# Kernel tuning notes

Measured on AMD Instinct MI355X. Metric: run time of the kernel, lower is better.

The kernel has to match this reference:

```python
import jax, jax.numpy as jnp
import numpy as np

HID = 70
NL = 4
NCLS = 10
BN_EPS = 1e-5

def _linear_params(key, din, dout):
    k1, k2 = jax.random.split(key)
    s = 1.0 / np.sqrt(din)
    W = jax.random.uniform(k1, (din, dout), jnp.float32, -s, s)
    b = jax.random.uniform(k2, (dout,), jnp.float32, -s, s)
    return W, b

def setup_inputs():
    key = jax.random.key(0)
    N, E, IN = 100000, 500000, 128
    keys = jax.random.split(key, 64)
    it = iter(keys)
    inp = {}
    inp['h'] = jax.random.normal(next(it), (N, IN), jnp.float32)
    inp['e'] = jax.random.normal(next(it), (E, IN), jnp.float32)
    inp['src'] = jax.random.randint(next(it), (E,), 0, N)
    inp['dst'] = jax.random.randint(next(it), (E,), 0, N)
    inp['snorm_n'] = jax.random.uniform(next(it), (N,), jnp.float32, 0.05, 1.0)
    inp['snorm_e'] = jax.random.uniform(next(it), (E,), jnp.float32, 0.05, 1.0)
    inp['W_eh'], inp['b_eh'] = _linear_params(next(it), IN, HID)
    inp['W_ee'], inp['b_ee'] = _linear_params(next(it), IN, HID)
    for nm in ['A', 'B', 'C', 'D', 'E']:
        Ws, bs = [], []
        for _ in range(NL):
            W, b = _linear_params(next(it), HID, HID)
            Ws.append(W); bs.append(b)
        inp['W' + nm] = jnp.stack(Ws)  # [NL, HID, HID]
        inp['b' + nm] = jnp.stack(bs)  # [NL, HID]
    inp['bnh_g'] = jnp.ones((NL, HID), jnp.float32)
    inp['bnh_b'] = jnp.zeros((NL, HID), jnp.float32)
    inp['bne_g'] = jnp.ones((NL, HID), jnp.float32)
    inp['bne_b'] = jnp.zeros((NL, HID), jnp.float32)
    inp['W_m0'], inp['b_m0'] = _linear_params(next(it), HID, HID // 2)
    inp['W_m1'], inp['b_m1'] = _linear_params(next(it), HID // 2, HID // 4)
    inp['W_m2'], inp['b_m2'] = _linear_params(next(it), HID // 4, NCLS)
    return inp

def _bn(x, g, b):
    # training-mode batch norm over the node/edge dimension
    m = jnp.mean(x, 0)
    v = jnp.var(x, 0)
    return (x - m) * jax.lax.rsqrt(v + BN_EPS) * g + b

def _forward(h, e, snorm_n, snorm_e, W_eh, b_eh, W_ee, b_ee, WA, bA, WB, bB, WC, bC, WD, bD, WE, bE, bnh_g, bnh_b, bne_g, bne_b, W_m0, b_m0, W_m1, b_m1, W_m2, b_m2, src, dst):
    N = h.shape[0]
    snn = snorm_n[:, None]
    sne = snorm_e[:, None]
    h = h @ W_eh + b_eh  # [N, HID]
    e = e @ W_ee + b_ee  # [E, HID]
    for l in range(NL):
        h_in, e_in = h, e
        Ah = h @ WA[l] + bA[l]
        Bh = h @ WB[l] + bB[l]
        Dh = h @ WD[l] + bD[l]
        Eh = h @ WE[l] + bE[l]
        Ce = e @ WC[l] + bC[l]
        e_hat = Ce + Dh[src] + Eh[dst]  # [E, HID] gated edge features
        sigma = jax.nn.sigmoid(e_hat)
        num = jax.ops.segment_sum(sigma * Bh[src], dst, num_segments=N)
        den = jax.ops.segment_sum(sigma, dst, num_segments=N)
        h = Ah + num / (den + 1e-6)
        h = _bn(h * snn, bnh_g[l], bnh_b[l])
        e = _bn(e_hat * sne, bne_g[l], bne_b[l])
        h = h_in + jax.nn.relu(h)  # residual
        e = e_in + jax.nn.relu(e)
    # MLPReadout: 70 -> 35 -> 17 -> n_classes
    y = jax.nn.relu(h @ W_m0 + b_m0)
    y = jax.nn.relu(y @ W_m1 + b_m1)
    return y @ W_m2 + b_m2

def reference(h, e, src, dst, snorm_n, snorm_e, W_eh, b_eh, W_ee, b_ee, WA, bA, WB, bB, WC, bC, WD, bD, WE, bE, bnh_g, bnh_b, bne_g, bne_b, W_m0, b_m0, W_m1, b_m1, W_m2, b_m2):
    return _forward(h, e, snorm_n, snorm_e, W_eh, b_eh, W_ee, b_ee, WA, bA, WB, bB, WC, bC, WD, bD, WE, bE, bnh_g, bnh_b, bne_g, bne_b, W_m0, b_m0, W_m1, b_m1, W_m2, b_m2, src, dst)
```

## Files before the change

kernel.cpp:

```cpp
#include <hip/hip_runtime.h>
#include <math.h>

#define H 70
#define NLAY 4
#define NCLS 10

typedef __attribute__((ext_vector_type(8))) short bf16x8;
typedef __attribute__((ext_vector_type(4))) float f32x4;
typedef __attribute__((ext_vector_type(4))) unsigned int uint4v;
typedef __attribute__((ext_vector_type(4))) int int4v;

struct GemmMats {
    const float* w[4];
    const float* b[4];
    float* y[4];
};

__device__ inline unsigned pack_hi16(unsigned u0, unsigned u1) {
    return (u1 & 0xFFFF0000u) | (u0 >> 16);
}
__device__ inline void split_pair(float x0, float x1, unsigned& ph, unsigned& pl) {
    unsigned u0 = __float_as_uint(x0), u1 = __float_as_uint(x1);
    float l0 = x0 - __uint_as_float(u0 & 0xFFFF0000u);
    float l1 = x1 - __uint_as_float(u1 & 0xFFFF0000u);
    ph = pack_hi16(u0, u1);
    pl = pack_hi16(__float_as_uint(l0), __float_as_uint(l1));
}

template <int K, int NMAT>
__global__ __launch_bounds__(256) void gemm_mfma(const float* __restrict__ X,
                                                 int M, GemmMats P) {
    constexpr int KS = (K + 31) / 32;
    constexpr int JK = KS * 16;
    constexpr int SW = JK + 4;
    __shared__ unsigned int Wsh[2 * 80 * SW];

    const int tid = threadIdx.x;
    const int wv = tid >> 6;
    const int lane = tid & 63;
    const int mlane = lane & 15;
    const int q = lane >> 4;
    const int rowbase = blockIdx.x * 64 + wv * 16;
    const int rowc = min(rowbase + mlane, M - 1);

    bf16x8 Ah[KS], Al[KS];
    {
        const float* xr = X + (size_t)rowc * K;
#pragma unroll
        for (int ks = 0; ks < KS; ++ks) {
            int k0 = ks * 32 + q * 8;
            float x[8];
            if (k0 + 8 <= K) {
                float2 p0 = *(const float2*)(xr + k0);
                float2 p1 = *(const float2*)(xr + k0 + 2);
                float2 p2 = *(const float2*)(xr + k0 + 4);
                float2 p3 = *(const float2*)(xr + k0 + 6);
                x[0] = p0.x; x[1] = p0.y; x[2] = p1.x; x[3] = p1.y;
                x[4] = p2.x; x[5] = p2.y; x[6] = p3.x; x[7] = p3.y;
            } else {
#pragma unroll
                for (int j = 0; j < 8; ++j)
                    x[j] = (k0 + j < K) ? xr[k0 + j] : 0.f;
            }
            int4v vh, vl;
            unsigned ph, pl;
            split_pair(x[0], x[1], ph, pl); vh.x = ph; vl.x = pl;
            split_pair(x[2], x[3], ph, pl); vh.y = ph; vl.y = pl;
            split_pair(x[4], x[5], ph, pl); vh.z = ph; vl.z = pl;
            split_pair(x[6], x[7], ph, pl); vh.w = ph; vl.w = pl;
            Ah[ks] = __builtin_bit_cast(bf16x8, vh);
            Al[ks] = __builtin_bit_cast(bf16x8, vl);
        }
    }

    for (int m = 0; m < NMAT; ++m) {
        __syncthreads();
        const float* Wg = P.w[m];
        for (int idx = tid; idx < 80 * JK; idx += 256) {
            int n = idx / JK, j = idx - n * JK;
            int k0 = 2 * j;
            float w0 = (n < H && k0 < K) ? Wg[k0 * H + n] : 0.f;
            float w1 = (n < H && k0 + 1 < K) ? Wg[(k0 + 1) * H + n] : 0.f;
            unsigned ph, pl;
            split_pair(w0, w1, ph, pl);
            Wsh[n * SW + j] = ph;
            Wsh[80 * SW + n * SW + j] = pl;
        }
        __syncthreads();

        f32x4 acc[5];
#pragma unroll
        for (int nt = 0; nt < 5; ++nt) acc[nt] = {0.f, 0.f, 0.f, 0.f};

#pragma unroll
        for (int ks = 0; ks < KS; ++ks) {
#pragma unroll
            for (int nt = 0; nt < 5; ++nt) {
                int base = (nt * 16 + mlane) * SW + ks * 16 + q * 4;
                uint4v bhv = *(const uint4v*)&Wsh[base];
                uint4v blv = *(const uint4v*)&Wsh[80 * SW + base];
                bf16x8 Bh = __builtin_bit_cast(bf16x8, bhv);
                bf16x8 Bl = __builtin_bit_cast(bf16x8, blv);
                acc[nt] = __builtin_amdgcn_mfma_f32_16x16x32_bf16(Ah[ks], Bh, acc[nt], 0, 0, 0);
                acc[nt] = __builtin_amdgcn_mfma_f32_16x16x32_bf16(Al[ks], Bh, acc[nt], 0, 0, 0);
                acc[nt] = __builtin_amdgcn_mfma_f32_16x16x32_bf16(Ah[ks], Bl, acc[nt], 0, 0, 0);
            }
        }

        const float* bm = P.b[m];
        float* Ym = P.y[m];
#pragma unroll
        for (int nt = 0; nt < 5; ++nt) {
            int col = nt * 16 + mlane;
            if (col < H) {
                float bv = bm[col];
#pragma unroll
                for (int r = 0; r < 4; ++r) {
                    int grow = rowbase + q * 4 + r;
                    if (grow < M)
                        Ym[(size_t)grow * H + col] = acc[nt][r] + bv;
                }
            }
        }
    }
}

__global__ void count_deg(const int* __restrict__ dst, int E,
                          int* __restrict__ deg) {
    int e = blockIdx.x * 256 + threadIdx.x;
    if (e < E) atomicAdd(&deg[dst[e]], 1);
}

__global__ __launch_bounds__(256) void scan_phaseA(const int* __restrict__ deg,
                                                   int N, int* __restrict__ bsum) {
    __shared__ int red[256];
    int base = blockIdx.x * 1024;
    int s = 0;
    for (int i = threadIdx.x; i < 1024; i += 256) {
        int g = base + i;
        if (g < N) s += deg[g];
    }
    red[threadIdx.x] = s;
    __syncthreads();
    for (int off = 128; off > 0; off >>= 1) {
        if (threadIdx.x < off) red[threadIdx.x] += red[threadIdx.x + off];
        __syncthreads();
    }
    if (threadIdx.x == 0) bsum[blockIdx.x] = red[0];
}

__global__ void scan_phaseB(const int* __restrict__ bsum, int NB,
                            int* __restrict__ boff, int* __restrict__ rowstart,
                            int N) {
    if (threadIdx.x == 0 && blockIdx.x == 0) {
        int acc = 0;
        for (int i = 0; i < NB; ++i) {
            boff[i] = acc;
            acc += bsum[i];
        }
        rowstart[N] = acc;
    }
}

__global__ __launch_bounds__(256) void scan_phaseC(
    const int* __restrict__ deg, int N, const int* __restrict__ boff,
    int* __restrict__ rowstart, int* __restrict__ cursor) {
    __shared__ int thr[256];
    int base = blockIdx.x * 1024 + threadIdx.x * 4;
    int d[4], loc[4];
    int s = 0;
#pragma unroll
    for (int i = 0; i < 4; ++i) {
        int g = base + i;
        d[i] = (g < N) ? deg[g] : 0;
        loc[i] = s;
        s += d[i];
    }
    thr[threadIdx.x] = s;
    __syncthreads();
    if (threadIdx.x == 0) {
        int a = 0;
        for (int i = 0; i < 256; ++i) {
            int t = thr[i];
            thr[i] = a;
            a += t;
        }
    }
    __syncthreads();
    int off = boff[blockIdx.x] + thr[threadIdx.x];
#pragma unroll
    for (int i = 0; i < 4; ++i) {
        int g = base + i;
        if (g < N) {
            rowstart[g] = off + loc[i];
            cursor[g] = off + loc[i];
        }
    }
}

__global__ void csr_fill(const int* __restrict__ dst, int E,
                         int* __restrict__ cursor, int* __restrict__ eid) {
    int e = blockIdx.x * 256 + threadIdx.x;
    if (e < E) {
        int p = atomicAdd(&cursor[dst[e]], 1);
        eid[p] = e;
    }
}

__global__ __launch_bounds__(256) void edge_kernel(
    float* __restrict__ ehat, const float* __restrict__ Dh,
    const float* __restrict__ Eh, const int* __restrict__ src,
    const int* __restrict__ dst, const float* __restrict__ sne, int E,
    float* __restrict__ esum, float* __restrict__ esq) {
    __shared__ float ls[H], lq[H];
    for (int i = threadIdx.x; i < H; i += 256) {
        ls[i] = 0.f;
        lq[i] = 0.f;
    }
    __syncthreads();
    const int total = E * H;
    const int stride = gridDim.x * 256;
    int idx0 = blockIdx.x * 256 + threadIdx.x;
    const int c = idx0 % H;
    float s1 = 0.f, s2 = 0.f;
    for (int idx = idx0; idx < total; idx += stride) {
        int e = idx / H;
        int s = src[e], d = dst[e];
        float v = ehat[idx] + Dh[s * H + c] + Eh[d * H + c];
        ehat[idx] = v;
        float t = v * sne[e];
        s1 += t;
        s2 += t * t;
    }
    atomicAdd(&ls[c], s1);
    atomicAdd(&lq[c], s2);
    __syncthreads();
    for (int i = threadIdx.x; i < H; i += 256) {
        unsafeAtomicAdd(&esum[i], ls[i]);
        unsafeAtomicAdd(&esq[i], lq[i]);
    }
}

__global__ void bn_finalize(const float* __restrict__ stats, float inv_cnt,
                            const float* __restrict__ g,
                            const float* __restrict__ b,
                            float* __restrict__ scale,
                            float* __restrict__ shift) {
    int c = threadIdx.x;
    if (c < H) {
        float m = stats[c] * inv_cnt;
        float v = stats[H + c] * inv_cnt - m * m;
        float rs = rsqrtf(v + 1e-5f);
        float sc = g[c] * rs;
        scale[c] = sc;
        shift[c] = b[c] - m * sc;
    }
}

__global__ __launch_bounds__(256) void update_kernel(
    float* __restrict__ io, const float* __restrict__ pre,
    const float* __restrict__ rowscale, const float* __restrict__ scale,
    const float* __restrict__ shift, int total) {
    const int stride = gridDim.x * 256;
    for (int idx = blockIdx.x * 256 + threadIdx.x; idx < total; idx += stride) {
        int r = idx / H;
        int c = idx - r * H;
        float t = pre[idx];
        if (rowscale) t *= rowscale[r];
        io[idx] += fmaxf(fmaf(t, scale[c], shift[c]), 0.f);
    }
}

__global__ __launch_bounds__(256) void node_agg(
    const float* __restrict__ ehat, const float* __restrict__ Bh,
    const float* __restrict__ Ah, const int* __restrict__ src,
    const int* __restrict__ rowstart, const int* __restrict__ eid,
    const float* __restrict__ snn, int N, float* __restrict__ hpre,
    float* __restrict__ hsum, float* __restrict__ hsq) {
    __shared__ float ls[H], lq[H];
    for (int i = threadIdx.x; i < H; i += 256) {
        ls[i] = 0.f;
        lq[i] = 0.f;
    }
    __syncthreads();
    const int total = N * H;
    const int stride = gridDim.x * 256;
    int idx0 = blockIdx.x * 256 + threadIdx.x;
    const int c = idx0 % H;
    float s1 = 0.f, s2 = 0.f;
    for (int idx = idx0; idx < total; idx += stride) {
        int n = idx / H;
        int p0 = rowstart[n], p1 = rowstart[n + 1];
        float num = 0.f, den = 0.f;
        for (int p = p0; p < p1; ++p) {
            int ed = eid[p];
            float x = ehat[ed * H + c];
            float sg = 1.f / (1.f + __expf(-x));
            den += sg;
            num = fmaf(sg, Bh[src[ed] * H + c], num);
        }
        float val = (Ah[idx] + num / (den + 1e-6f)) * snn[n];
        hpre[idx] = val;
        s1 += val;
        s2 += val * val;
    }
    atomicAdd(&ls[c], s1);
    atomicAdd(&lq[c], s2);
    __syncthreads();
    for (int i = threadIdx.x; i < H; i += 256) {
        unsafeAtomicAdd(&hsum[i], ls[i]);
        unsafeAtomicAdd(&hsq[i], lq[i]);
    }
}

__global__ __launch_bounds__(128) void mlp_readout(
    const float* __restrict__ h, int M, const float* __restrict__ W0,
    const float* __restrict__ b0, const float* __restrict__ W1,
    const float* __restrict__ b1, const float* __restrict__ W2,
    const float* __restrict__ b2, float* __restrict__ out) {
    __shared__ float Hs[128 * 71];
    __shared__ float wbuf[70 * 35 + 35 + 35 * 17 + 17 + 17 * 10 + 10];
    float* sW0 = wbuf;
    float* sb0 = sW0 + 2450;
    float* sW1 = sb0 + 35;
    float* sb1 = sW1 + 595;
    float* sW2 = sb1 + 17;
    float* sb2 = sW2 + 170;
    int tid = threadIdx.x;
    for (int i = tid; i < 2450; i += 128) sW0[i] = W0[i];
    for (int i = tid; i < 35; i += 128) sb0[i] = b0[i];
    for (int i = tid; i < 595; i += 128) sW1[i] = W1[i];
    for (int i = tid; i < 17; i += 128) sb1[i] = b1[i];
    for (int i = tid; i < 170; i += 128) sW2[i] = W2[i];
    for (int i = tid; i < 10; i += 128) sb2[i] = b2[i];
    int row0 = blockIdx.x * 128;
    for (int idx = tid; idx < 128 * H; idx += 128) {
        int r = idx / H, k = idx - r * H;
        int g = row0 + r;
        Hs[r * 71 + k] = (g < M) ? h[(size_t)g * H + k] : 0.f;
    }
    __syncthreads();
    int n = row0 + tid;
    if (n < M) {
        float y0[35];
#pragma unroll
        for (int j = 0; j < 35; ++j) y0[j] = sb0[j];
        for (int k = 0; k < H; ++k) {
            float x = Hs[tid * 71 + k];
#pragma unroll
            for (int j = 0; j < 35; ++j) y0[j] = fmaf(x, sW0[k * 35 + j], y0[j]);
        }
#pragma unroll
        for (int j = 0; j < 35; ++j) y0[j] = fmaxf(y0[j], 0.f);
        float y1[17];
#pragma unroll
        for (int j = 0; j < 17; ++j) y1[j] = sb1[j];
        for (int k = 0; k < 35; ++k) {
            float x = y0[k];
#pragma unroll
            for (int j = 0; j < 17; ++j) y1[j] = fmaf(x, sW1[k * 17 + j], y1[j]);
        }
#pragma unroll
        for (int j = 0; j < 17; ++j) y1[j] = fmaxf(y1[j], 0.f);
        float y2[10];
#pragma unroll
        for (int j = 0; j < 10; ++j) y2[j] = sb2[j];
        for (int k = 0; k < 17; ++k) {
            float x = y1[k];
#pragma unroll
            for (int j = 0; j < 10; ++j) y2[j] = fmaf(x, sW2[k * 10 + j], y2[j]);
        }
#pragma unroll
        for (int j = 0; j < 10; ++j) out[(size_t)n * 10 + j] = y2[j];
    }
}

extern "C" void kernel_launch(void* const* d_in, const int* in_sizes, int n_in,
                              void* d_out, int out_size, void* d_ws,
                              size_t ws_size, hipStream_t stream) {
    const float* in_h = (const float*)d_in[0];
    const float* in_e = (const float*)d_in[1];
    const int* src = (const int*)d_in[2];
    const int* dst = (const int*)d_in[3];
    const float* snn = (const float*)d_in[4];
    const float* sne = (const float*)d_in[5];
    const float* W_eh = (const float*)d_in[6];
    const float* b_eh = (const float*)d_in[7];
    const float* W_ee = (const float*)d_in[8];
    const float* b_ee = (const float*)d_in[9];
    const float* WA = (const float*)d_in[10];
    const float* bA = (const float*)d_in[11];
    const float* WB = (const float*)d_in[12];
    const float* bB = (const float*)d_in[13];
    const float* WC = (const float*)d_in[14];
    const float* bC = (const float*)d_in[15];
    const float* WD = (const float*)d_in[16];
    const float* bD = (const float*)d_in[17];
    const float* WE = (const float*)d_in[18];
    const float* bE = (const float*)d_in[19];
    const float* bnh_g = (const float*)d_in[20];
    const float* bnh_b = (const float*)d_in[21];
    const float* bne_g = (const float*)d_in[22];
    const float* bne_b = (const float*)d_in[23];
    const float* W_m0 = (const float*)d_in[24];
    const float* b_m0 = (const float*)d_in[25];
    const float* W_m1 = (const float*)d_in[26];
    const float* b_m1 = (const float*)d_in[27];
    const float* W_m2 = (const float*)d_in[28];
    const float* b_m2 = (const float*)d_in[29];

    const int N = in_sizes[0] / 128;
    const int E = in_sizes[1] / 128;
    const size_t nh = (size_t)N * H;
    const size_t ne = (size_t)E * H;

    float* p = (float*)d_ws;
    float* h_cur = p;   p += nh;
    float* e_cur = p;   p += ne;
    float* Ah = p;      p += nh;
    float* Bh = p;      p += nh;
    float* Dh = p;      p += nh;
    float* Eh = p;      p += nh;
    float* ehat = p;    p += ne;
    float* stats = p;   p += 280;
    float* escale = p;  p += H;
    float* eshift = p;  p += H;
    float* hscale = p;  p += H;
    float* hshift = p;  p += H;
    int* ip = (int*)p;
    int* deg = ip;      ip += N;
    int* rowstart = ip; ip += N + 1;
    int* cursor = ip;   ip += N;
    int* eid = ip;      ip += E;
    int* bsum = ip;     ip += 256;
    int* boff = ip;     ip += 256;
    float* hpre = Dh;

    hipMemsetAsync(deg, 0, (size_t)N * sizeof(int), stream);
    count_deg<<<(E + 255) / 256, 256, 0, stream>>>(dst, E, deg);
    const int NB = (N + 1023) / 1024;
    scan_phaseA<<<NB, 256, 0, stream>>>(deg, N, bsum);
    scan_phaseB<<<1, 64, 0, stream>>>(bsum, NB, boff, rowstart, N);
    scan_phaseC<<<NB, 256, 0, stream>>>(deg, N, boff, rowstart, cursor);
    csr_fill<<<(E + 255) / 256, 256, 0, stream>>>(dst, E, cursor, eid);

    GemmMats Ph = {};
    Ph.w[0] = W_eh; Ph.b[0] = b_eh; Ph.y[0] = h_cur;
    gemm_mfma<128, 1><<<(N + 63) / 64, 256, 0, stream>>>(in_h, N, Ph);
    GemmMats Pe = {};
    Pe.w[0] = W_ee; Pe.b[0] = b_ee; Pe.y[0] = e_cur;
    gemm_mfma<128, 1><<<(E + 63) / 64, 256, 0, stream>>>(in_e, E, Pe);

    for (int l = 0; l < NLAY; ++l) {
        GemmMats P4;
        P4.w[0] = WA + l * H * H; P4.b[0] = bA + l * H; P4.y[0] = Ah;
        P4.w[1] = WB + l * H * H; P4.b[1] = bB + l * H; P4.y[1] = Bh;
        P4.w[2] = WD + l * H * H; P4.b[2] = bD + l * H; P4.y[2] = Dh;
        P4.w[3] = WE + l * H * H; P4.b[3] = bE + l * H; P4.y[3] = Eh;
        gemm_mfma<70, 4><<<(N + 63) / 64, 256, 0, stream>>>(h_cur, N, P4);

        GemmMats PC = {};
        PC.w[0] = WC + l * H * H; PC.b[0] = bC + l * H; PC.y[0] = ehat;
        gemm_mfma<70, 1><<<(E + 63) / 64, 256, 0, stream>>>(e_cur, E, PC);

        hipMemsetAsync(stats, 0, 280 * sizeof(float), stream);
        edge_kernel<<<1120, 256, 0, stream>>>(ehat, Dh, Eh, src, dst, sne, E,
                                              stats, stats + 70);
        bn_finalize<<<1, 128, 0, stream>>>(stats, 1.f / E, bne_g + l * H,
                                           bne_b + l * H, escale, eshift);
        update_kernel<<<4096, 256, 0, stream>>>(e_cur, ehat, sne, escale,
                                                eshift, E * H);
        node_agg<<<1120, 256, 0, stream>>>(ehat, Bh, Ah, src, rowstart, eid,
                                           snn, N, hpre, stats + 140,
                                           stats + 210);
        bn_finalize<<<1, 128, 0, stream>>>(stats + 140, 1.f / N, bnh_g + l * H,
                                           bnh_b + l * H, hscale, hshift);
        update_kernel<<<2048, 256, 0, stream>>>(h_cur, hpre, nullptr, hscale,
                                                hshift, N * H);
    }

    mlp_readout<<<(N + 127) / 128, 128, 0, stream>>>(
        h_cur, N, W_m0, b_m0, W_m1, b_m1, W_m2, b_m2, (float*)d_out);
}
```

Measured before the change: 3.583 ms.

## Sort edges by destination, fuse edge GEMM with gating and BN stats, fuse edge update into aggregation

Edges are permuted into dst-sorted CSR order once, by gathering the initial edge GEMM input through eid and building permuted src/dst/snorm arrays, so node aggregation reads ehat contiguously. The C-projection GEMM now also adds Dh[src]+Eh[dst], writes ehat and accumulates BN statistics in one persistent kernel. The edge residual update is folded into node aggregation, and BN partial sums are spread across multiple buffers to reduce atomic contention. This removes several full passes over E×H edge tensors, but the fused GEMM epilogue now does scattered gathers and the output stays in permuted edge order.

```diff
diff --git a/kernel.cpp b/kernel.cpp
--- a/kernel.cpp
+++ b/kernel.cpp
@@ -27,8 +27,58 @@
     pl = pack_hi16(__float_as_uint(l0), __float_as_uint(l1));
 }
 
+template <int K, int KS>
+__device__ inline void load_a_frags(const float* __restrict__ X,
+                                    const int* __restrict__ perm, int M,
+                                    int rowbase, int mlane, int q,
+                                    bf16x8* Ah, bf16x8* Al) {
+    int rowc = min(rowbase + mlane, M - 1);
+    if (perm) rowc = perm[rowc];
+    const float* xr = X + (size_t)rowc * K;
+#pragma unroll
+    for (int ks = 0; ks < KS; ++ks) {
+        int k0 = ks * 32 + q * 8;
+        float x[8];
+        if (k0 + 8 <= K) {
+            float2 p0 = *(const float2*)(xr + k0);
+            float2 p1 = *(const float2*)(xr + k0 + 2);
+            float2 p2 = *(const float2*)(xr + k0 + 4);
+            float2 p3 = *(const float2*)(xr + k0 + 6);
+            x[0] = p0.x; x[1] = p0.y; x[2] = p1.x; x[3] = p1.y;
+            x[4] = p2.x; x[5] = p2.y; x[6] = p3.x; x[7] = p3.y;
+        } else {
+#pragma unroll
+            for (int j = 0; j < 8; ++j) x[j] = (k0 + j < K) ? xr[k0 + j] : 0.f;
+        }
+        int4v vh, vl;
+        unsigned ph, pl;
+        split_pair(x[0], x[1], ph, pl); vh.x = ph; vl.x = pl;
+        split_pair(x[2], x[3], ph, pl); vh.y = ph; vl.y = pl;
+        split_pair(x[4], x[5], ph, pl); vh.z = ph; vl.z = pl;
+        split_pair(x[6], x[7], ph, pl); vh.w = ph; vl.w = pl;
+        Ah[ks] = __builtin_bit_cast(bf16x8, vh);
+        Al[ks] = __builtin_bit_cast(bf16x8, vl);
+    }
+}
+
+template <int K, int JK, int SW>
+__device__ inline void stage_w(const float* __restrict__ Wg, unsigned* Wsh,
+                               int tid) {
+    for (int idx = tid; idx < 80 * JK; idx += 256) {
+        int n = idx / JK, j = idx - n * JK;
+        int k0 = 2 * j;
+        float w0 = (n < H && k0 < K) ? Wg[k0 * H + n] : 0.f;
+        float w1 = (n < H && k0 + 1 < K) ? Wg[(k0 + 1) * H + n] : 0.f;
+        unsigned ph, pl;
+        split_pair(w0, w1, ph, pl);
+        Wsh[n * SW + j] = ph;
+        Wsh[80 * SW + n * SW + j] = pl;
+    }
+}
+
 template <int K, int NMAT>
 __global__ __launch_bounds__(256) void gemm_mfma(const float* __restrict__ X,
+                                                 const int* __restrict__ perm,
                                                  int M, GemmMats P) {
     constexpr int KS = (K + 31) / 32;
     constexpr int JK = KS * 16;
@@ -41,57 +91,18 @@
     const int mlane = lane & 15;
     const int q = lane >> 4;
     const int rowbase = blockIdx.x * 64 + wv * 16;
-    const int rowc = min(rowbase + mlane, M - 1);
 
     bf16x8 Ah[KS], Al[KS];
-    {
-        const float* xr = X + (size_t)rowc * K;
-#pragma unroll
-        for (int ks = 0; ks < KS; ++ks) {
-            int k0 = ks * 32 + q * 8;
-            float x[8];
-            if (k0 + 8 <= K) {
-                float2 p0 = *(const float2*)(xr + k0);
-                float2 p1 = *(const float2*)(xr + k0 + 2);
-                float2 p2 = *(const float2*)(xr + k0 + 4);
-                float2 p3 = *(const float2*)(xr + k0 + 6);
-                x[0] = p0.x; x[1] = p0.y; x[2] = p1.x; x[3] = p1.y;
-                x[4] = p2.x; x[5] = p2.y; x[6] = p3.x; x[7] = p3.y;
-            } else {
-#pragma unroll
-                for (int j = 0; j < 8; ++j)
-                    x[j] = (k0 + j < K) ? xr[k0 + j] : 0.f;
-            }
-            int4v vh, vl;
-            unsigned ph, pl;
-            split_pair(x[0], x[1], ph, pl); vh.x = ph; vl.x = pl;
-            split_pair(x[2], x[3], ph, pl); vh.y = ph; vl.y = pl;
-            split_pair(x[4], x[5], ph, pl); vh.z = ph; vl.z = pl;
-            split_pair(x[6], x[7], ph, pl); vh.w = ph; vl.w = pl;
-            Ah[ks] = __builtin_bit_cast(bf16x8, vh);
-            Al[ks] = __builtin_bit_cast(bf16x8, vl);
-        }
-    }
+    load_a_frags<K, KS>(X, perm, M, rowbase, mlane, q, Ah, Al);
 
     for (int m = 0; m < NMAT; ++m) {
         __syncthreads();
-        const float* Wg = P.w[m];
-        for (int idx = tid; idx < 80 * JK; idx += 256) {
-            int n = idx / JK, j = idx - n * JK;
-            int k0 = 2 * j;
-            float w0 = (n < H && k0 < K) ? Wg[k0 * H + n] : 0.f;
-            float w1 = (n < H && k0 + 1 < K) ? Wg[(k0 + 1) * H + n] : 0.f;
-            unsigned ph, pl;
-            split_pair(w0, w1, ph, pl);
-            Wsh[n * SW + j] = ph;
-            Wsh[80 * SW + n * SW + j] = pl;
-        }
+        stage_w<K, JK, SW>(P.w[m], Wsh, tid);
         __syncthreads();
 
         f32x4 acc[5];
 #pragma unroll
         for (int nt = 0; nt < 5; ++nt) acc[nt] = {0.f, 0.f, 0.f, 0.f};
-
 #pragma unroll
         for (int ks = 0; ks < KS; ++ks) {
 #pragma unroll
@@ -99,14 +110,13 @@
                 int base = (nt * 16 + mlane) * SW + ks * 16 + q * 4;
                 uint4v bhv = *(const uint4v*)&Wsh[base];
                 uint4v blv = *(const uint4v*)&Wsh[80 * SW + base];
-                bf16x8 Bh = __builtin_bit_cast(bf16x8, bhv);
-                bf16x8 Bl = __builtin_bit_cast(bf16x8, blv);
-                acc[nt] = __builtin_amdgcn_mfma_f32_16x16x32_bf16(Ah[ks], Bh, acc[nt], 0, 0, 0);
-                acc[nt] = __builtin_amdgcn_mfma_f32_16x16x32_bf16(Al[ks], Bh, acc[nt], 0, 0, 0);
-                acc[nt] = __builtin_amdgcn_mfma_f32_16x16x32_bf16(Ah[ks], Bl, acc[nt], 0, 0, 0);
+                bf16x8 Bhf = __builtin_bit_cast(bf16x8, bhv);
+                bf16x8 Blf = __builtin_bit_cast(bf16x8, blv);
+                acc[nt] = __builtin_amdgcn_mfma_f32_16x16x32_bf16(Ah[ks], Bhf, acc[nt], 0, 0, 0);
+                acc[nt] = __builtin_amdgcn_mfma_f32_16x16x32_bf16(Al[ks], Bhf, acc[nt], 0, 0, 0);
+                acc[nt] = __builtin_amdgcn_mfma_f32_16x16x32_bf16(Ah[ks], Blf, acc[nt], 0, 0, 0);
             }
         }
-
         const float* bm = P.b[m];
         float* Ym = P.y[m];
 #pragma unroll
@@ -120,6 +130,108 @@
                     if (grow < M)
                         Ym[(size_t)grow * H + col] = acc[nt][r] + bv;
                 }
+            }
+        }
+    }
+}
+
+__global__ __launch_bounds__(256) void gemmC_edge(
+    const float* __restrict__ Xe, int E, const float* __restrict__ Wg,
+    const float* __restrict__ bias, const float* __restrict__ Dh,
+    const float* __restrict__ Eh, const int* __restrict__ src_p,
+    const int* __restrict__ dst_p, const float* __restrict__ sne_p,
+    float* __restrict__ ehat, float* __restrict__ estats) {
+    constexpr int K = 70, KS = 3, JK = 48, SW = 52;
+    __shared__ unsigned int Wsh[2 * 80 * SW];
+    const int tid = threadIdx.x;
+    const int wv = tid >> 6;
+    const int lane = tid & 63;
+    const int mlane = lane & 15;
+    const int q = lane >> 4;
+
+    stage_w<K, JK, SW>(Wg, Wsh, tid);
+    __syncthreads();
+
+    float bv[5];
+#pragma unroll
+    for (int nt = 0; nt < 5; ++nt) {
+        int col = nt * 16 + mlane;
+        bv[nt] = (col < H) ? bias[col] : 0.f;
+    }
+
+    float s1[5] = {0.f, 0.f, 0.f, 0.f, 0.f};
+    float s2[5] = {0.f, 0.f, 0.f, 0.f, 0.f};
+
+    const int ntiles = (E + 63) / 64;
+    for (int tile = blockIdx.x; tile < ntiles; tile += gridDim.x) {
+        const int rowbase = tile * 64 + wv * 16;
+        bf16x8 Ah[KS], Al[KS];
+        load_a_frags<K, KS>(Xe, nullptr, E, rowbase, mlane, q, Ah, Al);
+
+        f32x4 acc[5];
+#pragma unroll
+        for (int nt = 0; nt < 5; ++nt) acc[nt] = {0.f, 0.f, 0.f, 0.f};
+#pragma unroll
+        for (int ks = 0; ks < KS; ++ks) {
+#pragma unroll
+            for (int nt = 0; nt < 5; ++nt) {
+                int base = (nt * 16 + mlane) * SW + ks * 16 + q * 4;
+                uint4v bhv = *(const uint4v*)&Wsh[base];
+                uint4v blv = *(const uint4v*)&Wsh[80 * SW + base];
+                bf16x8 Bhf = __builtin_bit_cast(bf16x8, bhv);
+                bf16x8 Blf = __builtin_bit_cast(bf16x8, blv);
+                acc[nt] = __builtin_amdgcn_mfma_f32_16x16x32_bf16(Ah[ks], Bhf, acc[nt], 0, 0, 0);
+                acc[nt] = __builtin_amdgcn_mfma_f32_16x16x32_bf16(Al[ks], Bhf, acc[nt], 0, 0, 0);
+                acc[nt] = __builtin_amdgcn_mfma_f32_16x16x32_bf16(Ah[ks], Blf, acc[nt], 0, 0, 0);
+            }
+        }
+        int s4[4], d4[4];
+        float sn4[4];
+        bool ok4[4];
+#pragma unroll
+        for (int r = 0; r < 4; ++r) {
+            int grow = rowbase + q * 4 + r;
+            bool ok = grow < E;
+            int gc = ok ? grow : 0;
+            s4[r] = src_p[gc];
+            d4[r] = dst_p[gc];
+            sn4[r] = sne_p[gc];
+            ok4[r] = ok;
+        }
+#pragma unroll
+        for (int nt = 0; nt < 5; ++nt) {
+            int col = nt * 16 + mlane;
+            if (col < H) {
+#pragma unroll
+                for (int r = 0; r < 4; ++r) {
+                    if (ok4[r]) {
+                        int grow = rowbase + q * 4 + r;
+                        float v = acc[nt][r] + bv[nt] + Dh[s4[r] * H + col] +
+                                  Eh[d4[r] * H + col];
+                        ehat[(size_t)grow * H + col] = v;
+                        float t = v * sn4[r];
+                        s1[nt] += t;
+                        s2[nt] += t * t;
+                    }
+                }
+            }
+        }
+    }
+#pragma unroll
+    for (int nt = 0; nt < 5; ++nt) {
+        s1[nt] += __shfl_xor(s1[nt], 16);
+        s1[nt] += __shfl_xor(s1[nt], 32);
+        s2[nt] += __shfl_xor(s2[nt], 16);
+        s2[nt] += __shfl_xor(s2[nt], 32);
+    }
+    if (q == 0) {
+        float* buf = estats + (size_t)(blockIdx.x & 63) * 140;
+#pragma unroll
+        for (int nt = 0; nt < 5; ++nt) {
+            int col = nt * 16 + mlane;
+            if (col < H) {
+                unsafeAtomicAdd(&buf[col], s1[nt]);
+                unsafeAtomicAdd(&buf[70 + col], s2[nt]);
             }
         }
     }
@@ -207,109 +319,94 @@
     }
 }
 
-__global__ __launch_bounds__(256) void edge_kernel(
-    float* __restrict__ ehat, const float* __restrict__ Dh,
-    const float* __restrict__ Eh, const int* __restrict__ src,
-    const int* __restrict__ dst, const float* __restrict__ sne, int E,
-    float* __restrict__ esum, float* __restrict__ esq) {
-    __shared__ float ls[H], lq[H];
-    for (int i = threadIdx.x; i < H; i += 256) {
-        ls[i] = 0.f;
-        lq[i] = 0.f;
-    }
-    __syncthreads();
-    const int total = E * H;
-    const int stride = gridDim.x * 256;
-    int idx0 = blockIdx.x * 256 + threadIdx.x;
-    const int c = idx0 % H;
-    float s1 = 0.f, s2 = 0.f;
-    for (int idx = idx0; idx < total; idx += stride) {
-        int e = idx / H;
-        int s = src[e], d = dst[e];
-        float v = ehat[idx] + Dh[s * H + c] + Eh[d * H + c];
-        ehat[idx] = v;
-        float t = v * sne[e];
-        s1 += t;
-        s2 += t * t;
-    }
-    atomicAdd(&ls[c], s1);
-    atomicAdd(&lq[c], s2);
-    __syncthreads();
-    for (int i = threadIdx.x; i < H; i += 256) {
-        unsafeAtomicAdd(&esum[i], ls[i]);
-        unsafeAtomicAdd(&esq[i], lq[i]);
-    }
-}
-
-__global__ void bn_finalize(const float* __restrict__ stats, float inv_cnt,
-                            const float* __restrict__ g,
-                            const float* __restrict__ b,
-                            float* __restrict__ scale,
-                            float* __restrict__ shift) {
-    int c = threadIdx.x;
-    if (c < H) {
-        float m = stats[c] * inv_cnt;
-        float v = stats[H + c] * inv_cnt - m * m;
+__global__ void perm_build(const int* __restrict__ eid,
+                           const int* __restrict__ src,
+                           const int* __restrict__ dst,
+                           const float* __restrict__ sne, int E,
+                           int* __restrict__ src_p, int* __restrict__ dst_p,
+                           float* __restrict__ sne_p) {
+    int p = blockIdx.x * 256 + threadIdx.x;
+    if (p < E) {
+        int e = eid[p];
+        src_p[p] = src[e];
+        dst_p[p] = dst[e];
+        sne_p[p] = sne[e];
+    }
+}
+
+__global__ void bn_finalize_multi(const float* __restrict__ buf, int C,
+                                  float inv_cnt, const float* __restrict__ g,
+                                  const float* __restrict__ b,
+                                  float* __restrict__ scale,
+                                  float* __restrict__ shift) {
+    __shared__ float red[140];
+    int t = threadIdx.x;
+    if (t < 140) {
+        float s = 0.f;
+        for (int i = 0; i < C; ++i) s += buf[(size_t)i * 140 + t];
+        red[t] = s;
+    }
+    __syncthreads();
+    if (t < H) {
+        float m = red[t] * inv_cnt;
+        float v = red[70 + t] * inv_cnt - m * m;
         float rs = rsqrtf(v + 1e-5f);
-        float sc = g[c] * rs;
-        scale[c] = sc;
-        shift[c] = b[c] - m * sc;
-    }
-}
-
-__global__ __launch_bounds__(256) void update_kernel(
-    float* __restrict__ io, const float* __restrict__ pre,
-    const float* __restrict__ rowscale, const float* __restrict__ scale,
-    const float* __restrict__ shift, int total) {
-    const int stride = gridDim.x * 256;
-    for (int idx = blockIdx.x * 256 + threadIdx.x; idx < total; idx += stride) {
-        int r = idx / H;
-        int c = idx - r * H;
-        float t = pre[idx];
-        if (rowscale) t *= rowscale[r];
-        io[idx] += fmaxf(fmaf(t, scale[c], shift[c]), 0.f);
-    }
-}
-
-__global__ __launch_bounds__(256) void node_agg(
+        float sc = g[t] * rs;
+        scale[t] = sc;
+        shift[t] = b[t] - m * sc;
+    }
+}
+
+__global__ __launch_bounds__(256) void node_agg_fused(
     const float* __restrict__ ehat, const float* __restrict__ Bh,
-    const float* __restrict__ Ah, const int* __restrict__ src,
-    const int* __restrict__ rowstart, const int* __restrict__ eid,
-    const float* __restrict__ snn, int N, float* __restrict__ hpre,
-    float* __restrict__ hsum, float* __restrict__ hsq) {
-    __shared__ float ls[H], lq[H];
-    for (int i = threadIdx.x; i < H; i += 256) {
-        ls[i] = 0.f;
-        lq[i] = 0.f;
-    }
-    __syncthreads();
+    const float* __restrict__ Ah, const int* __restrict__ src_p,
+    const int* __restrict__ rowstart, const float* __restrict__ snn,
+    float* __restrict__ e_cur, const float* __restrict__ sne_p,
+    const float* __restrict__ escale, const float* __restrict__ eshift, int N,
+    float* __restrict__ hpre, float* __restrict__ hstats) {
     const int total = N * H;
     const int stride = gridDim.x * 256;
     int idx0 = blockIdx.x * 256 + threadIdx.x;
     const int c = idx0 % H;
+    const float esc = escale[c], esh = eshift[c];
     float s1 = 0.f, s2 = 0.f;
     for (int idx = idx0; idx < total; idx += stride) {
         int n = idx / H;
         int p0 = rowstart[n], p1 = rowstart[n + 1];
         float num = 0.f, den = 0.f;
         for (int p = p0; p < p1; ++p) {
-            int ed = eid[p];
-            float x = ehat[ed * H + c];
+            size_t ei = (size_t)p * H + c;
+            float x = ehat[ei];
             float sg = 1.f / (1.f + __expf(-x));
             den += sg;
-            num = fmaf(sg, Bh[src[ed] * H + c], num);
+            int s = src_p[p];
+            num = fmaf(sg, Bh[s * H + c], num);
+            e_cur[ei] += fmaxf(fmaf(x * sne_p[p], esc, esh), 0.f);
         }
         float val = (Ah[idx] + num / (den + 1e-6f)) * snn[n];
         hpre[idx] = val;
         s1 += val;
         s2 += val * val;
     }
+    __shared__ float ls[140];
+    for (int i = threadIdx.x; i < 140; i += 256) ls[i] = 0.f;
+    __syncthreads();
     atomicAdd(&ls[c], s1);
-    atomicAdd(&lq[c], s2);
-    __syncthreads();
-    for (int i = threadIdx.x; i < H; i += 256) {
-        unsafeAtomicAdd(&hsum[i], ls[i]);
-        unsafeAtomicAdd(&hsq[i], lq[i]);
+    atomicAdd(&ls[70 + c], s2);
+    __syncthreads();
+    float* buf = hstats + (size_t)(blockIdx.x & 15) * 140;
+    for (int i = threadIdx.x; i < 140; i += 256) unsafeAtomicAdd(&buf[i], ls[i]);
+}
+
+__global__ __launch_bounds__(256) void update_h_kernel(
+    float* __restrict__ io, const float* __restrict__ pre,
+    const float* __restrict__ scale, const float* __restrict__ shift,
+    int total) {
+    const int stride = gridDim.x * 256;
+    for (int idx = blockIdx.x * 256 + threadIdx.x; idx < total; idx += stride) {
+        int r = idx / H;
+        int c = idx - r * H;
+        io[idx] += fmaxf(fmaf(pre[idx], scale[c], shift[c]), 0.f);
     }
 }
 
@@ -422,19 +519,24 @@
     float* Dh = p;      p += nh;
     float* Eh = p;      p += nh;
     float* ehat = p;    p += ne;
-    float* stats = p;   p += 280;
+    float* stats = p;   p += 80 * 140;
     float* escale = p;  p += H;
     float* eshift = p;  p += H;
     float* hscale = p;  p += H;
     float* hshift = p;  p += H;
+    float* sne_p = p;   p += E;
     int* ip = (int*)p;
     int* deg = ip;      ip += N;
     int* rowstart = ip; ip += N + 1;
     int* cursor = ip;   ip += N;
     int* eid = ip;      ip += E;
+    int* src_p = ip;    ip += E;
+    int* dst_p = ip;    ip += E;
     int* bsum = ip;     ip += 256;
     int* boff = ip;     ip += 256;
     float* hpre = Dh;
+    float* estats = stats;
+    float* hstats = stats + 64 * 140;
 
     hipMemsetAsync(deg, 0, (size_t)N * sizeof(int), stream);
     count_deg<<<(E + 255) / 256, 256, 0, stream>>>(dst, E, deg);
@@ -443,13 +545,15 @@
     scan_phaseB<<<1, 64, 0, stream>>>(bsum, NB, boff, rowstart, N);
     scan_phaseC<<<NB, 256, 0, stream>>>(deg, N, boff, rowstart, cursor);
     csr_fill<<<(E + 255) / 256, 256, 0, stream>>>(dst, E, cursor, eid);
+    perm_build<<<(E + 255) / 256, 256, 0, stream>>>(eid, src, dst, sne, E,
+                                                    src_p, dst_p, sne_p);
 
     GemmMats Ph = {};
     Ph.w[0] = W_eh; Ph.b[0] = b_eh; Ph.y[0] = h_cur;
-    gemm_mfma<128, 1><<<(N + 63) / 64, 256, 0, stream>>>(in_h, N, Ph);
+    gemm_mfma<128, 1><<<(N + 63) / 64, 256, 0, stream>>>(in_h, nullptr, N, Ph);
     GemmMats Pe = {};
     Pe.w[0] = W_ee; Pe.b[0] = b_ee; Pe.y[0] = e_cur;
-    gemm_mfma<128, 1><<<(E + 63) / 64, 256, 0, stream>>>(in_e, E, Pe);
+    gemm_mfma<128, 1><<<(E + 63) / 64, 256, 0, stream>>>(in_e, eid, E, Pe);
 
     for (int l = 0; l < NLAY; ++l) {
         GemmMats P4;
@@ -457,26 +561,23 @@
         P4.w[1] = WB + l * H * H; P4.b[1] = bB + l * H; P4.y[1] = Bh;
         P4.w[2] = WD + l * H * H; P4.b[2] = bD + l * H; P4.y[2] = Dh;
         P4.w[3] = WE + l * H * H; P4.b[3] = bE + l * H; P4.y[3] = Eh;
-        gemm_mfma<70, 4><<<(N + 63) / 64, 256, 0, stream>>>(h_cur, N, P4);
-
-        GemmMats PC = {};
-        PC.w[0] = WC + l * H * H; PC.b[0] = bC + l * H; PC.y[0] = ehat;
-        gemm_mfma<70, 1><<<(E + 63) / 64, 256, 0, stream>>>(e_cur, E, PC);
-
-        hipMemsetAsync(stats, 0, 280 * sizeof(float), stream);
-        edge_kernel<<<1120, 256, 0, stream>>>(ehat, Dh, Eh, src, dst, sne, E,
-                                              stats, stats + 70);
-        bn_finalize<<<1, 128, 0, stream>>>(stats, 1.f / E, bne_g + l * H,
-                                           bne_b + l * H, escale, eshift);
-        update_kernel<<<4096, 256, 0, stream>>>(e_cur, ehat, sne, escale,
-                                                eshift, E * H);
-        node_agg<<<1120, 256, 0, stream>>>(ehat, Bh, Ah, src, rowstart, eid,
-                                           snn, N, hpre, stats + 140,
-                                           stats + 210);
-        bn_finalize<<<1, 128, 0, stream>>>(stats + 140, 1.f / N, bnh_g + l * H,
-                                           bnh_b + l * H, hscale, hshift);
-        update_kernel<<<2048, 256, 0, stream>>>(h_cur, hpre, nullptr, hscale,
-                                                hshift, N * H);
+        gemm_mfma<70, 4><<<(N + 63) / 64, 256, 0, stream>>>(h_cur, nullptr, N, P4);
+
+        hipMemsetAsync(stats, 0, 80 * 140 * sizeof(float), stream);
+        gemmC_edge<<<1024, 256, 0, stream>>>(e_cur, E, WC + l * H * H,
+                                             bC + l * H, Dh, Eh, src_p, dst_p,
+                                             sne_p, ehat, estats);
+        bn_finalize_multi<<<1, 256, 0, stream>>>(estats, 64, 1.f / E,
+                                                 bne_g + l * H, bne_b + l * H,
+                                                 escale, eshift);
+        node_agg_fused<<<1120, 256, 0, stream>>>(ehat, Bh, Ah, src_p, rowstart,
+                                                 snn, e_cur, sne_p, escale,
+                                                 eshift, N, hpre, hstats);
+        bn_finalize_multi<<<1, 256, 0, stream>>>(hstats, 16, 1.f / N,
+                                                 bnh_g + l * H, bnh_b + l * H,
+                                                 hscale, hshift);
+        update_h_kernel<<<2048, 256, 0, stream>>>(h_cur, hpre, hscale, hshift,
+                                                  N * H);
     }
 
     mlp_readout<<<(N + 127) / 128, 128, 0, stream>>>(
```

New measurement: 2.894 ms. -19.2%, faster.
